# Kernel tuning notes

Hardware: AMD Instinct MI355X
Metric: run time of the kernel (lower is better)

The kernel has to match this reference:

```python
import jax, jax.numpy as jnp
import numpy as np

N_WIRES = 4
N_LAYERS = 2
DIM = 2 ** N_WIRES  # 16
EPS = 1e-5

# PennyLane convention: wire 0 is the most-significant bit of the basis index.
def _bit(i, w):
    return (i >> (N_WIRES - 1 - w)) & 1

# CNOT(control=w, target=(w+1)%N_WIRES) as a basis-state permutation on [DIM]
def _cnot_perm(c, t):
    perm = np.arange(DIM)
    for i in range(DIM):
        if _bit(i, c) == 1:
            perm[i] = i ^ (1 << (N_WIRES - 1 - t))
    return jnp.asarray(perm)

CNOT_PERMS = [_cnot_perm(w, (w + 1) % N_WIRES) for w in range(N_WIRES)]

# PauliZ expectation signs: +1 if bit w of basis state is 0 else -1, shape [N_WIRES, DIM]
SIGNS = jnp.asarray(np.array([[1.0 - 2.0 * _bit(i, w) for i in range(DIM)]
                              for w in range(N_WIRES)], dtype=np.float32))

def _rx(t):
    c = jnp.cos(t / 2).astype(jnp.complex64)
    s = (-1j * jnp.sin(t / 2)).astype(jnp.complex64)
    return jnp.stack([jnp.stack([c, s], -1), jnp.stack([s, c], -1)], -2)

def _ry(t):
    c = jnp.cos(t / 2).astype(jnp.complex64)
    s = jnp.sin(t / 2).astype(jnp.complex64)
    return jnp.stack([jnp.stack([c, -s], -1), jnp.stack([s, c], -1)], -2)

def _rz(t):
    e0 = jnp.exp(-1j * t.astype(jnp.complex64) / 2)
    e1 = jnp.exp(1j * t.astype(jnp.complex64) / 2)
    z = jnp.zeros_like(e0)
    return jnp.stack([jnp.stack([e0, z], -1), jnp.stack([z, e1], -1)], -2)

def _apply1q(state, U, w):
    # state: [B, DIM] complex64; U: [2,2] (shared) or [B,2,2] (per-sample)
    B = state.shape[0]
    st = state.reshape(B, 2 ** w, 2, 2 ** (N_WIRES - 1 - w))
    if U.ndim == 3:
        st = jnp.einsum('blkr,bjk->bljr', st, U)
    else:
        st = jnp.einsum('blkr,jk->bljr', st, U)
    return st.reshape(B, DIM)

def _circuit(angles, weights):
    # angles: [B, N_WIRES] float32, weights: [N_LAYERS, N_WIRES, 3]
    B = angles.shape[0]
    state = jnp.zeros((B, DIM), jnp.complex64).at[:, 0].set(1.0)
    # AngleEmbedding: RX(angle) per wire (per-sample angles)
    for w in range(N_WIRES):
        state = _apply1q(state, _rx(angles[:, w]), w)
    for l in range(N_LAYERS):
        for w in range(N_WIRES):
            state = _apply1q(state, _rx(weights[l, w, 0]), w)
            state = _apply1q(state, _ry(weights[l, w, 1]), w)
            state = _apply1q(state, _rz(weights[l, w, 2]), w)
        for w in range(N_WIRES):
            state = state[:, CNOT_PERMS[w]]
    probs = state.real ** 2 + state.imag ** 2  # [B, DIM]
    return probs @ SIGNS.T  # [B, N_WIRES]

def setup_inputs() -> dict:
    key = jax.random.key(0)
    k1, k2 = jax.random.split(key)
    B = 131072
    x = jax.random.normal(k1, (B, 1, 12, 12), dtype=jnp.float32)
    weights = jax.random.normal(k2, (N_LAYERS, N_WIRES, 3), dtype=jnp.float32)
    gamma = jnp.ones((N_WIRES,), jnp.float32)
    beta = jnp.zeros((N_WIRES,), jnp.float32)
    return {"x": x, "weights": weights, "gamma": gamma, "beta": beta}

def reference(x, weights, gamma, beta):
    B = x.shape[0]
    # avg_pool2d(kernel=6, stride=6) on [B,1,12,12] -> [B,1,2,2] -> [B,4]
    pooled = x.reshape(B, 1, 2, 6, 2, 6).mean(axis=(3, 5)).reshape(B, N_WIRES)
    q = _circuit(pooled, weights)  # [B, 4]
    # dropout p=0 is identity; BatchNorm1d (training mode: batch stats, biased var)
    mean = q.mean(axis=0)
    var = q.var(axis=0)
    return (q - mean) / jnp.sqrt(var + EPS) * gamma + beta
```

## Files before the change

kernel.cpp:

```cpp
#include <hip/hip_runtime.h>

#define WS_SUMS   544
#define N_REP     8

__device__ __forceinline__ constexpr int tri(int i, int j){
  return 16*i - (i*(i-1))/2 + (j - i);
}

__global__ void k_pre(const float* __restrict__ W, float* __restrict__ ws){
  __shared__ float Ur[16][16];
  __shared__ float Uim[16][16];
  const int t = threadIdx.x;

  if (t < N_REP*8) ws[WS_SUMS + t] = 0.f;

  if (t < 16){
    float re[16], im[16];
    #pragma unroll
    for (int i = 0; i < 16; i++){ re[i] = 0.f; im[i] = 0.f; }
    re[t] = 1.f;

    #pragma unroll
    for (int l = 0; l < 2; l++){
      #pragma unroll
      for (int w = 0; w < 4; w++){
        const int m = 8 >> w;
        const float* g = W + (l*4 + w)*3;
        {
          float th = 0.5f*g[0], c = cosf(th), s = sinf(th);
          #pragma unroll
          for (int i0 = 0; i0 < 16; i0++) if (!(i0 & m)){
            int i1 = i0 | m;
            float a0r=re[i0], a0i=im[i0], a1r=re[i1], a1i=im[i1];
            re[i0] = c*a0r + s*a1i;  im[i0] = c*a0i - s*a1r;
            re[i1] = c*a1r + s*a0i;  im[i1] = c*a1i - s*a0r;
          }
        }
        {
          float th = 0.5f*g[1], c = cosf(th), s = sinf(th);
          #pragma unroll
          for (int i0 = 0; i0 < 16; i0++) if (!(i0 & m)){
            int i1 = i0 | m;
            float a0r=re[i0], a0i=im[i0], a1r=re[i1], a1i=im[i1];
            re[i0] = c*a0r - s*a1r;  im[i0] = c*a0i - s*a1i;
            re[i1] = s*a0r + c*a1r;  im[i1] = s*a0i + c*a1i;
          }
        }
        {
          float th = 0.5f*g[2], c = cosf(th), s = sinf(th);
          #pragma unroll
          for (int i0 = 0; i0 < 16; i0++) if (!(i0 & m)){
            int i1 = i0 | m;
            float a0r=re[i0], a0i=im[i0], a1r=re[i1], a1i=im[i1];
            re[i0] = c*a0r + s*a0i;  im[i0] = c*a0i - s*a0r;
            re[i1] = c*a1r - s*a1i;  im[i1] = c*a1i + s*a1r;
          }
        }
      }
      #pragma unroll
      for (int w = 0; w < 4; w++){
        const int mc = 8 >> w, mt = 8 >> ((w+1)&3);
        float nr[16], ni[16];
        #pragma unroll
        for (int i = 0; i < 16; i++){
          int src = (i & mc) ? (i ^ mt) : i;
          nr[i] = re[src]; ni[i] = im[src];
        }
        #pragma unroll
        for (int i = 0; i < 16; i++){ re[i] = nr[i]; im[i] = ni[i]; }
      }
    }
    #pragma unroll
    for (int k = 0; k < 16; k++){ Ur[k][t] = re[k]; Uim[k][t] = im[k]; }
  }
  __syncthreads();

  {
    const int i = t >> 4, j = t & 15;
    if (i <= j){
      const int d = (__popc(i) - __popc(j)) & 3;
      const int n = tri(i, j);
      #pragma unroll
      for (int w = 0; w < 4; w++){
        const int zm = 8 >> w;
        float mr = 0.f, mi = 0.f;
        #pragma unroll
        for (int k = 0; k < 16; k++){
          float z = (k & zm) ? -1.f : 1.f;
          float uir = Ur[k][i], uii = Uim[k][i];
          float ujr = Ur[k][j], uji = Uim[k][j];
          mr += z*(uir*ujr + uii*uji);
          mi += z*(uir*uji - uii*ujr);
        }
        float v = (d == 0) ? mr : (d == 1) ? -mi : (d == 2) ? -mr : mi;
        if (i != j) v *= 2.f;
        ws[n*4 + w] = v;
      }
    }
  }
}

__global__ __launch_bounds__(256) void k_main(const float* __restrict__ x,
                                              const float* __restrict__ A,
                                              float* __restrict__ qout,
                                              float* __restrict__ sums){
  __shared__ float wred[4][8];
  const int t = threadIdx.x;
  const size_t row = (size_t)blockIdx.x*256 + t;
  const float4* rp = (const float4*)(x + row*144);

  float aTL = 0.f, aTR = 0.f, aBL = 0.f, aBR = 0.f;
  #pragma unroll
  for (int ph = 0; ph < 3; ph++){
    float4 buf[12];
    #pragma unroll
    for (int j = 0; j < 12; j++) buf[j] = rp[ph*12 + j];
    #pragma unroll
    for (int j = 0; j < 12; j++){
      const int p  = ph*12 + j;
      const int cg = p % 3;
      float s01 = buf[j].x + buf[j].y, s23 = buf[j].z + buf[j].w;
      float L = (cg == 0) ? (s01 + s23) : ((cg == 1) ? s01 : 0.f);
      float R = (cg == 2) ? (s01 + s23) : ((cg == 1) ? s23 : 0.f);
      if (p < 18){ aTL += L; aTR += R; } else { aBL += L; aBR += R; }
    }
  }

  const float inv = 1.f/72.f;
  float s0,c0,s1,c1,s2,c2,s3,c3;
  __sincosf(aTL*inv, &s0, &c0);
  __sincosf(aTR*inv, &s1, &c1);
  __sincosf(aBL*inv, &s2, &c2);
  __sincosf(aBR*inv, &s3, &c3);

  float t00=c0*c1, t01=c0*s1, t10=s0*c1, t11=s0*s1;
  float u00=c2*c3, u01=c2*s3, u10=s2*c3, u11=s2*s3;
  float r[16];
  r[ 0]=t00*u00; r[ 1]=t00*u01; r[ 2]=t00*u10; r[ 3]=t00*u11;
  r[ 4]=t01*u00; r[ 5]=t01*u01; r[ 6]=t01*u10; r[ 7]=t01*u11;
  r[ 8]=t10*u00; r[ 9]=t10*u01; r[10]=t10*u10; r[11]=t10*u11;
  r[12]=t11*u00; r[13]=t11*u01; r[14]=t11*u10; r[15]=t11*u11;

  float q0=0.f, q1=0.f, q2=0.f, q3=0.f;
  #pragma unroll
  for (int i = 0; i < 16; i++){
    #pragma unroll
    for (int j = i; j < 16; j++){
      const int n = tri(i, j);
      float pij = r[i]*r[j];
      q0 = fmaf(A[n*4+0], pij, q0);
      q1 = fmaf(A[n*4+1], pij, q1);
      q2 = fmaf(A[n*4+2], pij, q2);
      q3 = fmaf(A[n*4+3], pij, q3);
    }
  }

  ((float4*)qout)[row] = make_float4(q0, q1, q2, q3);

  float red[8] = {q0, q1, q2, q3, q0*q0, q1*q1, q2*q2, q3*q3};
  #pragma unroll
  for (int off = 32; off >= 1; off >>= 1){
    #pragma unroll
    for (int k = 0; k < 8; k++) red[k] += __shfl_down(red[k], off, 64);
  }
  const int lane = t & 63, wv = t >> 6;
  if (lane == 0){
    #pragma unroll
    for (int k = 0; k < 8; k++) wred[wv][k] = red[k];
  }
  __syncthreads();
  if (t < 8){
    float s = wred[0][t] + wred[1][t] + wred[2][t] + wred[3][t];
    atomicAdd(&sums[(blockIdx.x & (N_REP-1))*8 + t], s);
  }
}

__global__ __launch_bounds__(256) void k_statsnorm(float* __restrict__ out,
                                                   const float* __restrict__ sums,
                                                   const float* __restrict__ gamma,
                                                   const float* __restrict__ beta,
                                                   float invB){
  const int idx = blockIdx.x*256 + threadIdx.x;
  float sc[4], sh[4];
  #pragma unroll
  for (int w = 0; w < 4; w++){
    float s1 = 0.f, s2 = 0.f;
    #pragma unroll
    for (int rep = 0; rep < N_REP; rep++){
      s1 += sums[rep*8 + w];
      s2 += sums[rep*8 + 4 + w];
    }
    float mean  = s1 * invB;
    float var   = s2 * invB - mean*mean;
    float scale = gamma[w] * rsqrtf(var + 1e-5f);
    sc[w] = scale;
    sh[w] = fmaf(-mean, scale, beta[w]);
  }
  float4* o4 = (float4*)out;
  float4 qv = o4[idx];
  qv.x = fmaf(qv.x, sc[0], sh[0]);
  qv.y = fmaf(qv.y, sc[1], sh[1]);
  qv.z = fmaf(qv.z, sc[2], sh[2]);
  qv.w = fmaf(qv.w, sc[3], sh[3]);
  o4[idx] = qv;
}

extern "C" void kernel_launch(void* const* d_in, const int* in_sizes, int n_in,
                              void* d_out, int out_size, void* d_ws, size_t ws_size,
                              hipStream_t stream){
  const float* x     = (const float*)d_in[0];
  const float* W     = (const float*)d_in[1];
  const float* gamma = (const float*)d_in[2];
  const float* beta  = (const float*)d_in[3];
  float* ws  = (float*)d_ws;
  float* out = (float*)d_out;
  const int B = in_sizes[0] / 144;

  k_pre<<<1, 256, 0, stream>>>(W, ws);
  k_main<<<B/256, 256, 0, stream>>>(x, ws, out, ws + WS_SUMS);
  k_statsnorm<<<B/256, 256, 0, stream>>>(out, ws + WS_SUMS, gamma, beta, 1.f/(float)B);
}
```

Measured before the change: 131.8 us.

## Fuse main pass and batch-norm into one cooperative kernel with grid sync

Merges the per-row circuit evaluation and the batch-norm normalization into a single kernel launched cooperatively. A grid-wide sync sits between the atomic accumulation of batch sums and the normalization. Each thread keeps its four q values in registers, so the intermediate q array is never written out and re-read, and one kernel launch goes away. The cost is a grid-wide barrier, plus the requirement that all 512 blocks be co-resident, which launch_bounds(256,2) is meant to make possible.

```diff
diff --git a/kernel.cpp b/kernel.cpp
--- a/kernel.cpp
+++ b/kernel.cpp
@@ -1,4 +1,7 @@
 #include <hip/hip_runtime.h>
+#include <hip/hip_cooperative_groups.h>
+
+namespace cg = cooperative_groups;
 
 #define WS_SUMS   544
 #define N_REP     8
@@ -100,10 +103,13 @@
   }
 }
 
-__global__ __launch_bounds__(256) void k_main(const float* __restrict__ x,
-                                              const float* __restrict__ A,
-                                              float* __restrict__ qout,
-                                              float* __restrict__ sums){
+__global__ __launch_bounds__(256, 2) void k_fused(const float* __restrict__ x,
+                                                  const float* __restrict__ A,
+                                                  float* __restrict__ out,
+                                                  float* sums,
+                                                  const float* __restrict__ gamma,
+                                                  const float* __restrict__ beta,
+                                                  float invB){
   __shared__ float wred[4][8];
   const int t = threadIdx.x;
   const size_t row = (size_t)blockIdx.x*256 + t;
@@ -155,8 +161,6 @@
     }
   }
 
-  ((float4*)qout)[row] = make_float4(q0, q1, q2, q3);
-
   float red[8] = {q0, q1, q2, q3, q0*q0, q1*q1, q2*q2, q3*q3};
   #pragma unroll
   for (int off = 32; off >= 1; off >>= 1){
@@ -173,36 +177,31 @@
     float s = wred[0][t] + wred[1][t] + wred[2][t] + wred[3][t];
     atomicAdd(&sums[(blockIdx.x & (N_REP-1))*8 + t], s);
   }
-}
-
-__global__ __launch_bounds__(256) void k_statsnorm(float* __restrict__ out,
-                                                   const float* __restrict__ sums,
-                                                   const float* __restrict__ gamma,
-                                                   const float* __restrict__ beta,
-                                                   float invB){
-  const int idx = blockIdx.x*256 + threadIdx.x;
+
+  cg::this_grid().sync();
+
   float sc[4], sh[4];
   #pragma unroll
   for (int w = 0; w < 4; w++){
-    float s1 = 0.f, s2 = 0.f;
+    float s1v = 0.f, s2v = 0.f;
     #pragma unroll
     for (int rep = 0; rep < N_REP; rep++){
-      s1 += sums[rep*8 + w];
-      s2 += sums[rep*8 + 4 + w];
-    }
-    float mean  = s1 * invB;
-    float var   = s2 * invB - mean*mean;
+      s1v += __hip_atomic_load(&sums[rep*8 + w],     __ATOMIC_RELAXED, __HIP_MEMORY_SCOPE_AGENT);
+      s2v += __hip_atomic_load(&sums[rep*8 + 4 + w], __ATOMIC_RELAXED, __HIP_MEMORY_SCOPE_AGENT);
+    }
+    float mean  = s1v * invB;
+    float var   = s2v * invB - mean*mean;
     float scale = gamma[w] * rsqrtf(var + 1e-5f);
     sc[w] = scale;
     sh[w] = fmaf(-mean, scale, beta[w]);
   }
-  float4* o4 = (float4*)out;
-  float4 qv = o4[idx];
-  qv.x = fmaf(qv.x, sc[0], sh[0]);
-  qv.y = fmaf(qv.y, sc[1], sh[1]);
-  qv.z = fmaf(qv.z, sc[2], sh[2]);
-  qv.w = fmaf(qv.w, sc[3], sh[3]);
-  o4[idx] = qv;
+
+  float4 qv;
+  qv.x = fmaf(q0, sc[0], sh[0]);
+  qv.y = fmaf(q1, sc[1], sh[1]);
+  qv.z = fmaf(q2, sc[2], sh[2]);
+  qv.w = fmaf(q3, sc[3], sh[3]);
+  ((float4*)out)[row] = qv;
 }
 
 extern "C" void kernel_launch(void* const* d_in, const int* in_sizes, int n_in,
@@ -217,6 +216,12 @@
   const int B = in_sizes[0] / 144;
 
   k_pre<<<1, 256, 0, stream>>>(W, ws);
-  k_main<<<B/256, 256, 0, stream>>>(x, ws, out, ws + WS_SUMS);
-  k_statsnorm<<<B/256, 256, 0, stream>>>(out, ws + WS_SUMS, gamma, beta, 1.f/(float)B);
-}
+
+  const float* A   = ws;
+  float* sums      = ws + WS_SUMS;
+  float invB       = 1.f/(float)B;
+  void* args[] = { (void*)&x, (void*)&A, (void*)&out, (void*)&sums,
+                   (void*)&gamma, (void*)&beta, (void*)&invB };
+  hipLaunchCooperativeKernel((const void*)k_fused, dim3(B/256), dim3(256),
+                             args, 0, stream);
+}
```

Measured after the change: 218.0 us. 1.65x slower.

## Fuse unitary precompute into main kernel and replace atomics with per-block partials

Applied to the files above, without the earlier changes.

Removes the separate single-block precompute launch. Every block of the main kernel now recomputes the 16x16 circuit unitary and the observable coefficient table into shared memory, overlapping that work with its global loads of x, and reads the coefficients as float4 from LDS instead of from global memory. Atomic accumulation into replicated sum slots is replaced by per-block partial writes, which every block of the normalization kernel re-reduces (512 blocks × 8 floats). This saves a launch and the zero-init, at the cost of redundant per-block trig and unitary work and a redundant partial reduction in each stats block.

```diff
diff --git a/kernel.cpp b/kernel.cpp
--- a/kernel.cpp
+++ b/kernel.cpp
@@ -1,18 +1,21 @@
 #include <hip/hip_runtime.h>
 
-#define WS_SUMS   544
-#define N_REP     8
 
 __device__ __forceinline__ constexpr int tri(int i, int j){
   return 16*i - (i*(i-1))/2 + (j - i);
 }
 
-__global__ void k_pre(const float* __restrict__ W, float* __restrict__ ws){
+__global__ __launch_bounds__(256) void k_main(const float* __restrict__ x,
+                                              const float* __restrict__ W,
+                                              float* __restrict__ qout,
+                                              float* __restrict__ partials){
   __shared__ float Ur[16][16];
   __shared__ float Uim[16][16];
+  __shared__ float As[544];
+  __shared__ float wred[4][8];
   const int t = threadIdx.x;
-
-  if (t < N_REP*8) ws[WS_SUMS + t] = 0.f;
+  const size_t row = (size_t)blockIdx.x*256 + t;
+  const float4* rp = (const float4*)(x + row*144);
 
   if (t < 16){
     float re[16], im[16];
@@ -73,6 +76,24 @@
     #pragma unroll
     for (int k = 0; k < 16; k++){ Ur[k][t] = re[k]; Uim[k][t] = im[k]; }
   }
+
+  float aTL = 0.f, aTR = 0.f, aBL = 0.f, aBR = 0.f;
+  #pragma unroll
+  for (int ph = 0; ph < 3; ph++){
+    float4 buf[12];
+    #pragma unroll
+    for (int j = 0; j < 12; j++) buf[j] = rp[ph*12 + j];
+    #pragma unroll
+    for (int j = 0; j < 12; j++){
+      const int p  = ph*12 + j;
+      const int cg = p % 3;
+      float s01 = buf[j].x + buf[j].y, s23 = buf[j].z + buf[j].w;
+      float L = (cg == 0) ? (s01 + s23) : ((cg == 1) ? s01 : 0.f);
+      float R = (cg == 2) ? (s01 + s23) : ((cg == 1) ? s23 : 0.f);
+      if (p < 18){ aTL += L; aTR += R; } else { aBL += L; aBR += R; }
+    }
+  }
+
   __syncthreads();
 
   {
@@ -94,37 +115,11 @@
         }
         float v = (d == 0) ? mr : (d == 1) ? -mi : (d == 2) ? -mr : mi;
         if (i != j) v *= 2.f;
-        ws[n*4 + w] = v;
+        As[n*4 + w] = v;
       }
     }
   }
-}
-
-__global__ __launch_bounds__(256) void k_main(const float* __restrict__ x,
-                                              const float* __restrict__ A,
-                                              float* __restrict__ qout,
-                                              float* __restrict__ sums){
-  __shared__ float wred[4][8];
-  const int t = threadIdx.x;
-  const size_t row = (size_t)blockIdx.x*256 + t;
-  const float4* rp = (const float4*)(x + row*144);
-
-  float aTL = 0.f, aTR = 0.f, aBL = 0.f, aBR = 0.f;
-  #pragma unroll
-  for (int ph = 0; ph < 3; ph++){
-    float4 buf[12];
-    #pragma unroll
-    for (int j = 0; j < 12; j++) buf[j] = rp[ph*12 + j];
-    #pragma unroll
-    for (int j = 0; j < 12; j++){
-      const int p  = ph*12 + j;
-      const int cg = p % 3;
-      float s01 = buf[j].x + buf[j].y, s23 = buf[j].z + buf[j].w;
-      float L = (cg == 0) ? (s01 + s23) : ((cg == 1) ? s01 : 0.f);
-      float R = (cg == 2) ? (s01 + s23) : ((cg == 1) ? s23 : 0.f);
-      if (p < 18){ aTL += L; aTR += R; } else { aBL += L; aBR += R; }
-    }
-  }
+  __syncthreads();
 
   const float inv = 1.f/72.f;
   float s0,c0,s1,c1,s2,c2,s3,c3;
@@ -146,12 +141,12 @@
   for (int i = 0; i < 16; i++){
     #pragma unroll
     for (int j = i; j < 16; j++){
-      const int n = tri(i, j);
+      const float4 a4 = *(const float4*)&As[tri(i, j)*4];
       float pij = r[i]*r[j];
-      q0 = fmaf(A[n*4+0], pij, q0);
-      q1 = fmaf(A[n*4+1], pij, q1);
-      q2 = fmaf(A[n*4+2], pij, q2);
-      q3 = fmaf(A[n*4+3], pij, q3);
+      q0 = fmaf(a4.x, pij, q0);
+      q1 = fmaf(a4.y, pij, q1);
+      q2 = fmaf(a4.z, pij, q2);
+      q3 = fmaf(a4.w, pij, q3);
     }
   }
 
@@ -171,31 +166,52 @@
   __syncthreads();
   if (t < 8){
     float s = wred[0][t] + wred[1][t] + wred[2][t] + wred[3][t];
-    atomicAdd(&sums[(blockIdx.x & (N_REP-1))*8 + t], s);
-  }
-}
-
-__global__ __launch_bounds__(256) void k_statsnorm(float* __restrict__ out,
-                                                   const float* __restrict__ sums,
-                                                   const float* __restrict__ gamma,
-                                                   const float* __restrict__ beta,
-                                                   float invB){
-  const int idx = blockIdx.x*256 + threadIdx.x;
+    partials[blockIdx.x*8 + t] = s;
+  }
+}
+
+__global__ __launch_bounds__(256) void k_stats(float* __restrict__ out,
+                                               const float* __restrict__ partials,
+                                               const float* __restrict__ gamma,
+                                               const float* __restrict__ beta,
+                                               float invB, int nb){
+  __shared__ float wred[4][8];
+  __shared__ float tot[8];
+  const int t = threadIdx.x;
+
+  float red[8] = {0.f,0.f,0.f,0.f,0.f,0.f,0.f,0.f};
+  const float4* p4 = (const float4*)partials;
+  for (int b = t; b < nb; b += 256){
+    float4 A0 = p4[b*2+0];
+    float4 A1 = p4[b*2+1];
+    red[0] += A0.x; red[1] += A0.y; red[2] += A0.z; red[3] += A0.w;
+    red[4] += A1.x; red[5] += A1.y; red[6] += A1.z; red[7] += A1.w;
+  }
+  #pragma unroll
+  for (int off = 32; off >= 1; off >>= 1){
+    #pragma unroll
+    for (int k = 0; k < 8; k++) red[k] += __shfl_down(red[k], off, 64);
+  }
+  const int lane = t & 63, wv = t >> 6;
+  if (lane == 0){
+    #pragma unroll
+    for (int k = 0; k < 8; k++) wred[wv][k] = red[k];
+  }
+  __syncthreads();
+  if (t < 8) tot[t] = wred[0][t] + wred[1][t] + wred[2][t] + wred[3][t];
+  __syncthreads();
+
   float sc[4], sh[4];
   #pragma unroll
   for (int w = 0; w < 4; w++){
-    float s1 = 0.f, s2 = 0.f;
-    #pragma unroll
-    for (int rep = 0; rep < N_REP; rep++){
-      s1 += sums[rep*8 + w];
-      s2 += sums[rep*8 + 4 + w];
-    }
-    float mean  = s1 * invB;
-    float var   = s2 * invB - mean*mean;
+    float mean  = tot[w] * invB;
+    float var   = tot[4+w] * invB - mean*mean;
     float scale = gamma[w] * rsqrtf(var + 1e-5f);
     sc[w] = scale;
     sh[w] = fmaf(-mean, scale, beta[w]);
   }
+
+  const int idx = blockIdx.x*256 + t;
   float4* o4 = (float4*)out;
   float4 qv = o4[idx];
   qv.x = fmaf(qv.x, sc[0], sh[0]);
@@ -214,9 +230,9 @@
   const float* beta  = (const float*)d_in[3];
   float* ws  = (float*)d_ws;
   float* out = (float*)d_out;
-  const int B = in_sizes[0] / 144;
-
-  k_pre<<<1, 256, 0, stream>>>(W, ws);
-  k_main<<<B/256, 256, 0, stream>>>(x, ws, out, ws + WS_SUMS);
-  k_statsnorm<<<B/256, 256, 0, stream>>>(out, ws + WS_SUMS, gamma, beta, 1.f/(float)B);
-}
+  const int B  = in_sizes[0] / 144;
+  const int nb = B / 256;
+
+  k_main <<<nb, 256, 0, stream>>>(x, W, out, ws);
+  k_stats<<<nb, 256, 0, stream>>>(out, ws, gamma, beta, 1.f/(float)B, nb);
+}
```

Result: faster. 120.7 us (-8.5%).
